# Kernel optimization log

Measured on AMD Instinct MI355X. Metric: run time of the kernel, lower is better.

## Reference

```python
import jax, jax.numpy as jnp
import numpy as np

B, N_SRC, N_NGH, D, H = 256, 32, 2048, 128, 2
DK = D // H  # 64
FEAT = 128
NEG_INF = -1e10
LN_EPS = 1e-5


def setup_inputs() -> dict:
    key = jax.random.key(0)
    ks = jax.random.split(key, 16)
    inp = {
        "src": jax.random.normal(ks[0], (B, N_SRC, D), jnp.float32),
        "ngh_feat": jax.random.normal(ks[1], (B * N_NGH, D), jnp.float32),
        "hidden": jnp.zeros((B * N_NGH, D), jnp.float32),
        "mask": jax.random.bernoulli(ks[2], 0.5, (B, N_NGH)),
        # GRUCell params (torch layout: [3H, in], gate order r,z,n)
        "gru_w_ih": jax.random.normal(ks[3], (3 * D, D), jnp.float32) * 0.05,
        "gru_w_hh": jax.random.normal(ks[4], (3 * D, D), jnp.float32) * 0.05,
        "gru_b_ih": jnp.zeros((3 * D,), jnp.float32),
        "gru_b_hh": jnp.zeros((3 * D,), jnp.float32),
        # multi-head attention projections (no bias in source)
        "w_qs": jax.random.normal(ks[5], (H * DK, D), jnp.float32) * np.sqrt(2.0 / (D + DK)).astype(np.float32),
        "w_ks": jax.random.normal(ks[6], (H * DK, D), jnp.float32) * np.sqrt(2.0 / (D + DK)).astype(np.float32),
        "w_vs": jax.random.normal(ks[7], (H * DK, D), jnp.float32) * np.sqrt(2.0 / (D + DK)).astype(np.float32),
        "fc_w": jax.random.normal(ks[8], (D, H * DK), jnp.float32) * 0.05,
        "fc_b": jnp.zeros((D,), jnp.float32),
        "ln_g": jnp.ones((D,), jnp.float32),
        "ln_b": jnp.zeros((D,), jnp.float32),
        # MergeLayer(model_dim, model_dim, feat_dim, feat_dim)
        "m_fc1_w": jax.random.normal(ks[9], (FEAT, 2 * D), jnp.float32) * 0.05,
        "m_fc1_b": jnp.zeros((FEAT,), jnp.float32),
        "m_fc2_w": jax.random.normal(ks[10], (FEAT, FEAT), jnp.float32) * 0.05,
        "m_fc2_b": jnp.zeros((FEAT,), jnp.float32),
    }
    return inp


def gru_cell(x, h, w_ih, w_hh, b_ih, b_hh):
    gi = x @ w_ih.T + b_ih
    gh = h @ w_hh.T + b_hh
    ir, iz, in_ = jnp.split(gi, 3, axis=-1)
    hr, hz, hn = jnp.split(gh, 3, axis=-1)
    r = jax.nn.sigmoid(ir + hr)
    z = jax.nn.sigmoid(iz + hz)
    n = jnp.tanh(in_ + r * hn)
    return (1.0 - z) * n + z * h


def reference(src, ngh_feat, hidden, mask,
              gru_w_ih, gru_w_hh, gru_b_ih, gru_b_hh,
              w_qs, w_ks, w_vs, fc_w, fc_b, ln_g, ln_b,
              m_fc1_w, m_fc1_b, m_fc2_w, m_fc2_b):
    b, n_src, d = src.shape
    n_ngh = mask.shape[1]
    nn = n_ngh // n_src  # neighbors per source
    temperature = jnp.sqrt(jnp.float32(DK))

    # GRU walk encoding of neighbor features -> seq [B, N_ngh, D]
    seq = gru_cell(ngh_feat, hidden, gru_w_ih, gru_w_hh, gru_b_ih, gru_b_hh)
    seq = seq.reshape(b, n_ngh, d)

    # grouped multi-head attention (q per source, k/v over its nn neighbors)
    q = (src @ w_qs.T).reshape(b, n_src, H, DK)            # bshd
    k = (seq @ w_ks.T).reshape(b, n_src, nn, H, DK)        # bsnhd
    v = (seq @ w_vs.T).reshape(b, n_src, nn, H, DK)
    scores = jnp.einsum('bshd,bsnhd->bshn', q, k) / temperature
    m = mask.reshape(b, n_src, 1, nn)                      # broadcast over heads
    scores = jnp.where(m, NEG_INF, scores)
    attn = jax.nn.softmax(scores, axis=-1)                 # dropout is eval no-op
    out = jnp.einsum('bshn,bsnhd->bshd', attn, v).reshape(b, n_src, H * DK)
    out = out @ fc_w.T + fc_b

    # residual + layernorm
    x = out + src
    mu = jnp.mean(x, axis=-1, keepdims=True)
    var = jnp.var(x, axis=-1, keepdims=True)
    x = (x - mu) * jax.lax.rsqrt(var + LN_EPS) * ln_g + ln_b

    # MergeLayer: cat + MLP
    cat = jnp.concatenate([x, src], axis=-1)
    h1 = jax.nn.relu(cat @ m_fc1_w.T + m_fc1_b)
    z = h1 @ m_fc2_w.T + m_fc2_b                            # [B, N_src, feat_dim]
    return z
```

## Files before the change

kernel.cpp:

```cpp
#include <hip/hip_runtime.h>

typedef float  f32x4  __attribute__((ext_vector_type(4)));
typedef short  bf16x8 __attribute__((ext_vector_type(8)));
typedef unsigned short u16x4 __attribute__((ext_vector_type(4)));

typedef const __attribute__((address_space(1))) unsigned int* gas_u32;
typedef __attribute__((address_space(3))) unsigned int* las_u32;

#define MFMA16(a,b,c) __builtin_amdgcn_mfma_f32_16x16x32_bf16((a),(b),(c),0,0,0)

__device__ __forceinline__ unsigned short f2bf(float f){
  unsigned u = __float_as_uint(f);
  u += 0x7fffu + ((u>>16)&1u);
  return (unsigned short)(u>>16);
}
__device__ __forceinline__ float bf2f(unsigned short u){
  return __uint_as_float(((unsigned)u)<<16);
}
__device__ __forceinline__ float sigm(float x){
  return __fdividef(1.f, 1.f + __expf(-x));
}
__device__ __forceinline__ float tanhfast(float x){
  return 1.f - __fdividef(2.f, __expf(2.f*x) + 1.f);
}
__device__ __forceinline__ float dot128(const float* __restrict__ w, const float* s){
  float a0=0.f,a1=0.f,a2=0.f,a3=0.f;
  #pragma unroll
  for (int e=0;e<32;++e){
    f32x4 w4 = *(const f32x4*)(w + (e<<2));
    f32x4 x4 = *(const f32x4*)(s + (e<<2));
    a0 = fmaf(w4[0],x4[0],a0); a1 = fmaf(w4[1],x4[1],a1);
    a2 = fmaf(w4[2],x4[2],a2); a3 = fmaf(w4[3],x4[3],a3);
  }
  return (a0+a1)+(a2+a3);
}
__device__ __forceinline__ bf16x8 cvt8(const f32x4 a, const f32x4 b){
  union { int i[4]; bf16x8 v; } u;
  asm("v_cvt_pk_bf16_f32 %0, %1, %2" : "=v"(u.i[0]) : "v"(a[0]), "v"(a[1]));
  asm("v_cvt_pk_bf16_f32 %0, %1, %2" : "=v"(u.i[1]) : "v"(a[2]), "v"(a[3]));
  asm("v_cvt_pk_bf16_f32 %0, %1, %2" : "=v"(u.i[2]) : "v"(b[0]), "v"(b[1]));
  asm("v_cvt_pk_bf16_f32 %0, %1, %2" : "=v"(u.i[3]) : "v"(b[2]), "v"(b[3]));
  return u.v;
}
__device__ __forceinline__ int swx(int m){ return (((m&7)<<1) | ((m>>3)&1)) << 2; }
__device__ __forceinline__ int sws(int m){ return ((m&7)<<3) | (((m>>3)&1)<<6); }

#define XB_OFF   0
#define SEQ_OFF  32768
#define QK_OFF   49152
#define SC_OFF   53248
#define SH_OFF   53760
#define BIAS_OFF 57856
#define SMEM_SZ  59904

__global__ void prep_all(const float* __restrict__ wih, const float* __restrict__ whh,
                         const float* __restrict__ wqs, const float* __restrict__ wks,
                         const float* __restrict__ wvs, const float* __restrict__ fcw,
                         const float* __restrict__ src, const int* __restrict__ mask_i,
                         const float* __restrict__ hid,
                         unsigned short* __restrict__ wbf, float* __restrict__ M_ws,
                         unsigned short* __restrict__ qk_ws,
                         unsigned long long* __restrict__ mask_bits,
                         int* __restrict__ flags){
  __shared__ __align__(16) float sl_src[32*128];
  __shared__ __align__(16) float sl_q[32*128];
  const int b = blockIdx.x, t = threadIdx.x;
  if (b < 384){
    const int tid = b*256 + t;
    if (tid < 49152) wbf[tid] = f2bf(wih[tid]);
    else             wbf[tid] = f2bf(whh[tid-49152]);
  } else if (b < 512){
    const int tid = (b-384)*256 + t;
    const int h = tid>>14, d = (tid>>7)&127, e = tid&127;
    float a = 0.f;
    for (int j=0;j<64;++j)
      a = fmaf(fcw[d*128 + (h<<6) + j], wvs[((h<<6)+j)*128 + e], a);
    M_ws[tid] = a;
  } else if (b < 768){
    const int blk = b - 512;
    const size_t s0 = (size_t)blk * 32;
    for (int i=0;i<16;++i) sl_src[t + i*256] = src[s0*128 + t + i*256];
    __syncthreads();
    for (int k=0;k<16;++k){
      const int job = t + k*256, s = job>>7, c = job&127;
      sl_q[job] = dot128(wqs + c*128, sl_src + s*128);
    }
    __syncthreads();
    const int d = t&127, h = (t>>7)&1;
    float acc[32];
    #pragma unroll
    for (int s=0;s<32;++s) acc[s]=0.f;
    for (int j=0;j<64;++j){
      const float wk = wks[((h<<6)+j)*128 + d];
      #pragma unroll
      for (int s=0;s<32;++s) acc[s] = fmaf(wk, sl_q[s*128 + (h<<6) + j], acc[s]);
    }
    for (int s=0;s<32;++s) qk_ws[(s0+s)*256 + (h<<7) + d] = f2bf(acc[s]);
  } else if (b < 2816){
    const int blk = b - 768;
    const int wv = t>>6, lane = t&63;
    const int gsrc = blk*4 + wv;
    const unsigned v = (unsigned)mask_i[(size_t)gsrc*64 + lane];
    const int bytemode = __any((int)(v > 1u));
    bool bit;
    if (bytemode) bit = (((const unsigned char*)mask_i)[(size_t)gsrc*64 + lane] != 0);
    else          bit = (v != 0u);
    const unsigned long long bits = __ballot((int)bit);
    if (lane == 0) mask_bits[gsrc] = bits;
  } else {
    const size_t blk = b - 2816;
    bool nz = false;
    #pragma unroll 4
    for (int it=0; it<32; ++it){
      const size_t idx = blk*8192 + (size_t)it*256 + t;
      const f32x4 v = *(const f32x4*)(hid + idx*4);
      nz = nz || (v[0]!=0.f)||(v[1]!=0.f)||(v[2]!=0.f)||(v[3]!=0.f);
    }
    if (__ballot((int)nz)){ if ((t&63)==0) atomicOr(flags+1, 1); }
  }
}

__device__ __forceinline__ void scores_pv(char* smem, int srcI, unsigned long long mb,
                                          int wv, int lane){
  const unsigned short* seq = (const unsigned short*)(smem + SEQ_OFF);
  const float* qk_lds = (const float*)(smem + QK_OFF);
  float* sc = (float*)(smem + SC_OFF);
  float* sH = (float*)(smem + SH_OFF);
  {
    const int hh = wv & 1;
    const float* qrow = qk_lds + (srcI<<8) + (hh<<7);
    float a = 0.f;
    #pragma unroll
    for (int c8=0; c8<16; ++c8){
      const int cb = c8<<3;
      bf16x8 kc = *(const bf16x8*)&seq[(lane<<7) + (cb ^ sws(lane))];
      #pragma unroll
      for (int u=0;u<8;++u) a = fmaf(bf2f((unsigned short)kc[u]), qrow[cb+u], a);
    }
    float s = ((mb>>lane)&1ull) ? -1e10f : a*0.125f;
    float mx = s;
    #pragma unroll
    for (int o=32;o>=1;o>>=1) mx = fmaxf(mx, __shfl_xor(mx,o));
    const float e = __expf(s - mx);
    float sum = e;
    #pragma unroll
    for (int o=32;o>=1;o>>=1) sum += __shfl_xor(sum,o);
    if (wv < 2) sc[(hh<<6)+lane] = __fdividef(e, sum);
  }
  asm volatile("s_waitcnt lgkmcnt(0)" ::: "memory");
  __builtin_amdgcn_sched_barrier(0);
  __builtin_amdgcn_s_barrier();
  {
    const int tt = (wv<<6)+lane;
    const int jidx = tt>>2, sub = tt&3;
    const int hh2 = jidx>>5, quad = jidx&31;
    f32x4 a = {0.f,0.f,0.f,0.f};
    #pragma unroll
    for (int i=0;i<16;++i){
      const int rr = (sub<<4)+i;
      const u16x4 sv = *(const u16x4*)&seq[(rr<<7) + ((quad<<2) ^ sws(rr))];
      const float w = sc[(hh2<<6)+rr];
      #pragma unroll
      for (int k=0;k<4;++k) a[k] = fmaf(w, bf2f(sv[k]), a[k]);
    }
    #pragma unroll
    for (int k=0;k<4;++k) a[k] += __shfl_xor(a[k],1);
    #pragma unroll
    for (int k=0;k<4;++k) a[k] += __shfl_xor(a[k],2);
    if (sub == 0)
      *(f32x4*)&sH[(((srcI<<1)+hh2)<<7) + (quad<<2)] = a;
  }
}

__global__ __attribute__((amdgpu_flat_work_group_size(256,256)))
           __attribute__((amdgpu_waves_per_eu(2)))
void cawn_main(
    const float* __restrict__ src, const float* __restrict__ ngh,
    const float* __restrict__ hid,
    const float* __restrict__ bih, const float* __restrict__ bhh,
    const float* __restrict__ fcb, const float* __restrict__ lng,
    const float* __restrict__ lnb, const float* __restrict__ m1w,
    const float* __restrict__ m1b, const float* __restrict__ m2w,
    const float* __restrict__ m2b,
    const unsigned short* __restrict__ wihb, const unsigned short* __restrict__ whhb,
    const float* __restrict__ M_ws, const unsigned short* __restrict__ qk_ws,
    const unsigned long long* __restrict__ mask_bits,
    const int* __restrict__ flags, float* __restrict__ out)
{
  __shared__ __align__(16) char smem[SMEM_SZ];
  float* qk_lds = (float*)(smem + QK_OFF);
  float* brz0   = (float*)(smem + BIAS_OFF);
  float* brz1   = (float*)(smem + BIAS_OFF + 512);
  float* bin_l  = (float*)(smem + BIAS_OFF + 1024);
  float* bhn_l  = (float*)(smem + BIAS_OFF + 1536);
  unsigned short* seq = (unsigned short*)(smem + SEQ_OFF);

  const int t    = threadIdx.x;
  const int wv   = t >> 6;
  const int lane = t & 63;
  const int l15  = lane & 15;
  const int lgrp = lane >> 4;
  const int gsrc0 = blockIdx.x * 4;
  const f32x4 z4 = {0.f,0.f,0.f,0.f};
  const int hz = flags[1];

  if (t < 128){
    brz0[t]  = bih[t]     + bhh[t];
    brz1[t]  = bih[128+t] + bhh[128+t];
    bin_l[t] = bih[256+t];
    bhn_l[t] = bhh[256+t];
  }
  #pragma unroll
  for (int s=0;s<4;++s)
    qk_lds[(s<<8)+t] = bf2f(qk_ws[(size_t)(gsrc0+s)*256 + t]);
  const unsigned long long mb0 = mask_bits[gsrc0];
  const unsigned long long mb1 = mask_bits[gsrc0+1];
  const unsigned long long mb2 = mask_bits[gsrc0+2];
  const unsigned long long mb3 = mask_bits[gsrc0+3];

  if (!hz){
    bf16x8 Wf[3][2][4];
    #pragma unroll
    for (int g=0; g<3; ++g)
      #pragma unroll
      for (int j=0; j<2; ++j){
        const int nc = (wv<<5) + (j<<4) + l15;
        #pragma unroll
        for (int kb=0; kb<4; ++kb)
          Wf[g][j][kb] = *(const bf16x8*)(wihb + (((g<<7) + nc)<<7) + (kb<<5) + (lgrp<<3));
      }

    auto issue = [&](int kk){
      const int srcI = kk>>2, stg = kk&3;
      const size_t base = (size_t)(gsrc0+srcI)*8192 + (size_t)stg*2048;
      #pragma unroll
      for (int r=0;r<2;++r){
        const int rl = (wv<<2) + (r<<1) + (lane>>5);
        const int s16 = (lane&31) ^ (((rl&7)<<1) | ((rl>>3)&1));
        const float* g = ngh + base + (rl<<7) + (s16<<2);
        char* l = smem + XB_OFF + (kk&3)*8192 + (((wv<<2)+(r<<1))<<9);
        __builtin_amdgcn_global_load_lds((gas_u32)g, (las_u32)l, 16, 0, 0);
      }
    };
    issue(0); issue(1);

    for (int k=0;k<16;++k){
      if (k < 14) issue(k+2);
      if (k < 14)      asm volatile("s_waitcnt vmcnt(4) lgkmcnt(0)" ::: "memory");
      else if (k==14)  asm volatile("s_waitcnt vmcnt(2) lgkmcnt(0)" ::: "memory");
      else             asm volatile("s_waitcnt vmcnt(0) lgkmcnt(0)" ::: "memory");
      __builtin_amdgcn_sched_barrier(0);
      __builtin_amdgcn_s_barrier();

      const int srcI = k>>2, stg = k&3;
      const float* xrow = (const float*)(smem + XB_OFF + (k&3)*8192) + (l15<<7);
      const int sw = swx(l15);
      bf16x8 bx[4];
      #pragma unroll
      for (int kb=0;kb<4;++kb){
        const int c0 = (kb<<5) + (lgrp<<3);
        const f32x4 u0 = *(const f32x4*)&xrow[c0 ^ sw];
        const f32x4 u1 = *(const f32x4*)&xrow[(c0+4) ^ sw];
        bx[kb] = cvt8(u0,u1);
      }
      f32x4 ar[2]={z4,z4}, az[2]={z4,z4}, an[2]={z4,z4};
      #pragma unroll
      for (int j=0;j<2;++j)
        #pragma unroll
        for (int kb=0;kb<4;++kb){
          ar[j] = MFMA16(Wf[0][j][kb], bx[kb], ar[j]);
          az[j] = MFMA16(Wf[1][j][kb], bx[kb], az[j]);
          an[j] = MFMA16(Wf[2][j][kb], bx[kb], an[j]);
        }
      const int mrow = (stg<<4) + l15;
      #pragma unroll
      for (int j=0;j<2;++j){
        const int colb = (wv<<5) + (j<<4) + (lgrp<<2);
        const f32x4 b0 = *(const f32x4*)&brz0[colb];
        const f32x4 b1 = *(const f32x4*)&brz1[colb];
        const f32x4 b2 = *(const f32x4*)&bin_l[colb];
        const f32x4 b3 = *(const f32x4*)&bhn_l[colb];
        u16x4 sq;
        #pragma unroll
        for (int i=0;i<4;++i){
          const float rv = sigm(ar[j][i] + b0[i]);
          const float zv = sigm(az[j][i] + b1[i]);
          const float nv = tanhfast(an[j][i] + b2[i] + rv*b3[i]);
          sq[i] = f2bf((1.f - zv)*nv);
        }
        *(u16x4*)&seq[(mrow<<7) + (colb ^ sws(mrow))] = sq;
      }

      if (stg == 3){
        asm volatile("s_waitcnt lgkmcnt(0)" ::: "memory");
        __builtin_amdgcn_sched_barrier(0);
        __builtin_amdgcn_s_barrier();
        const unsigned long long mb = (srcI==0)?mb0:(srcI==1)?mb1:(srcI==2)?mb2:mb3;
        scores_pv(smem, srcI, mb, wv, lane);
      }
    }
  } else {
    float* xb0 = (float*)(smem + XB_OFF);
    float* xb1 = (float*)(smem + XB_OFF + 8192);
    for (int srcI=0;srcI<4;++srcI){
      const int gsrc = gsrc0+srcI;
      for (int stg=0;stg<4;++stg){
        #pragma unroll
        for (int it=0; it<2; ++it){
          const int f = t + (it<<8);
          const int m = f>>5, c0 = (f&31)<<2;
          const int sw = swx(m);
          const size_t gb = (size_t)gsrc*8192 + stg*2048 + (m<<7) + c0;
          *(f32x4*)&xb0[(m<<7)+(c0^sw)] = *(const f32x4*)(ngh+gb);
          *(f32x4*)&xb1[(m<<7)+(c0^sw)] = *(const f32x4*)(hid+gb);
        }
        __syncthreads();
        const float* xrow = xb0 + (l15<<7);
        const float* hrow = xb1 + (l15<<7);
        const int sw = swx(l15);
        bf16x8 bx[4], bh[4];
        #pragma unroll
        for (int kb=0;kb<4;++kb){
          const int c0 = (kb<<5) + (lgrp<<3);
          bx[kb] = cvt8(*(const f32x4*)&xrow[c0 ^ sw], *(const f32x4*)&xrow[(c0+4) ^ sw]);
          bh[kb] = cvt8(*(const f32x4*)&hrow[c0 ^ sw], *(const f32x4*)&hrow[(c0+4) ^ sw]);
        }
        f32x4 ar[2]={z4,z4}, az[2]={z4,z4}, an[2]={z4,z4}, anh[2]={z4,z4};
        #pragma unroll
        for (int j=0;j<2;++j){
          const int nc = (wv<<5)+(j<<4)+l15;
          #pragma unroll
          for (int kb=0;kb<4;++kb){
            const int ko=(kb<<5)+(lgrp<<3);
            bf16x8 w0 = *(const bf16x8*)(wihb + ((      nc)<<7) + ko);
            bf16x8 w1 = *(const bf16x8*)(wihb + (((128)+nc)<<7) + ko);
            bf16x8 w2 = *(const bf16x8*)(wihb + (((256)+nc)<<7) + ko);
            ar[j] = MFMA16(w0, bx[kb], ar[j]);
            az[j] = MFMA16(w1, bx[kb], az[j]);
            an[j] = MFMA16(w2, bx[kb], an[j]);
            bf16x8 u0 = *(const bf16x8*)(whhb + ((      nc)<<7) + ko);
            bf16x8 u1 = *(const bf16x8*)(whhb + (((128)+nc)<<7) + ko);
            bf16x8 u2 = *(const bf16x8*)(whhb + (((256)+nc)<<7) + ko);
            ar[j]  = MFMA16(u0, bh[kb], ar[j]);
            az[j]  = MFMA16(u1, bh[kb], az[j]);
            anh[j] = MFMA16(u2, bh[kb], anh[j]);
          }
        }
        const int mrow = (stg<<4) + l15;
        #pragma unroll
        for (int j=0;j<2;++j){
          const int colb = (wv<<5) + (j<<4) + (lgrp<<2);
          const f32x4 b0 = *(const f32x4*)&brz0[colb];
          const f32x4 b1 = *(const f32x4*)&brz1[colb];
          const f32x4 b2 = *(const f32x4*)&bin_l[colb];
          const f32x4 b3 = *(const f32x4*)&bhn_l[colb];
          const f32x4 hv = *(const f32x4*)&hrow[colb ^ sw];
          u16x4 sq;
          #pragma unroll
          for (int i=0;i<4;++i){
            const float rv = sigm(ar[j][i] + b0[i]);
            const float zv = sigm(az[j][i] + b1[i]);
            const float nv = tanhfast(an[j][i] + b2[i] + rv*(anh[j][i] + b3[i]));
            sq[i] = f2bf((1.f - zv)*nv + zv*hv[i]);
          }
          *(u16x4*)&seq[(mrow<<7) + (colb ^ sws(mrow))] = sq;
        }
        __syncthreads();
      }
      const unsigned long long mb = (srcI==0)?mb0:(srcI==1)?mb1:(srcI==2)?mb2:mb3;
      scores_pv(smem, srcI, mb, wv, lane);
      __syncthreads();
    }
  }

  __syncthreads();
  float* ep1  = (float*)smem;
  float* ep2  = (float*)(smem + 2048);
  float* srce = (float*)(smem + 4096);
  float* sH   = (float*)(smem + SH_OFF);
  srce[t]     = src[(size_t)gsrc0*128 + t];
  srce[t+256] = src[(size_t)gsrc0*128 + t + 256];
  __syncthreads();

  const int d  = t & 127;
  const int sh = (t >> 7) << 1;
  #pragma unroll
  for (int si=0; si<2; ++si){
    const int s = sh + si;
    float a = fcb[d];
    a += dot128(M_ws +         d*128, &sH[((s<<1)  )<<7]);
    a += dot128(M_ws + 16384 + d*128, &sH[((s<<1)+1)<<7]);
    ep1[s*128+d] = a + srce[s*128+d];
  }
  __syncthreads();
  {
    const int s = wv;
    const float v0 = ep1[s*128+lane], v1 = ep1[s*128+64+lane];
    float sum = v0+v1, sq_ = v0*v0 + v1*v1;
    #pragma unroll
    for (int o=32;o>=1;o>>=1){ sum += __shfl_xor(sum,o); sq_ += __shfl_xor(sq_,o); }
    const float mu  = sum * 0.0078125f;
    const float var = sq_ * 0.0078125f - mu*mu;
    const float rs  = rsqrtf(var + 1e-5f);
    ep1[s*128+lane]    = (v0-mu)*rs*lng[lane]    + lnb[lane];
    ep1[s*128+64+lane] = (v1-mu)*rs*lng[64+lane] + lnb[64+lane];
  }
  __syncthreads();
  #pragma unroll
  for (int si=0; si<2; ++si){
    const int s = sh + si;
    float a = m1b[d];
    a += dot128(m1w + d*256,       ep1  + s*128);
    a += dot128(m1w + d*256 + 128, srce + s*128);
    ep2[s*128+d] = fmaxf(a, 0.f);
  }
  __syncthreads();
  #pragma unroll
  for (int si=0; si<2; ++si){
    const int s = sh + si;
    out[(size_t)(gsrc0+s)*128 + d] = m2b[d] + dot128(m2w + d*128, ep2 + s*128);
  }
}

extern "C" void kernel_launch(void* const* d_in, const int* in_sizes, int n_in,
                              void* d_out, int out_size, void* d_ws, size_t ws_size,
                              hipStream_t stream){
  const float* src = (const float*)d_in[0];
  const float* ngh = (const float*)d_in[1];
  const float* hid = (const float*)d_in[2];
  const int*   msk = (const int*)  d_in[3];
  const float* wih = (const float*)d_in[4];
  const float* whh = (const float*)d_in[5];
  const float* bih = (const float*)d_in[6];
  const float* bhh = (const float*)d_in[7];
  const float* wqs = (const float*)d_in[8];
  const float* wks = (const float*)d_in[9];
  const float* wvs = (const float*)d_in[10];
  const float* fcw = (const float*)d_in[11];
  const float* fcb = (const float*)d_in[12];
  const float* lng = (const float*)d_in[13];
  const float* lnb = (const float*)d_in[14];
  const float* m1w = (const float*)d_in[15];
  const float* m1b = (const float*)d_in[16];
  const float* m2w = (const float*)d_in[17];
  const float* m2b = (const float*)d_in[18];
  float* out = (float*)d_out;

  unsigned short* wbf   = (unsigned short*)d_ws;
  int*            flags = (int*)((char*)d_ws + 196608);
  float*          M_ws  = (float*)((char*)d_ws + 196672);
  unsigned short* qk_ws = (unsigned short*)((char*)d_ws + 327744);
  unsigned long long* mask_bits = (unsigned long long*)((char*)d_ws + 4522048);

  hipMemsetAsync((char*)d_ws + 196608, 0, 64, stream);
  prep_all <<<4864, 256, 0, stream>>>(wih, whh, wqs, wks, wvs, fcw, src, msk, hid,
                                      wbf, M_ws, qk_ws, mask_bits, flags);
  cawn_main<<<2048, 256, 0, stream>>>(src, ngh, hid, bih, bhh,
                                      fcb, lng, lnb, m1w, m1b, m2w, m2b,
                                      wbf, wbf + 49152, M_ws, qk_ws,
                                      mask_bits, flags, out);
}
```

Baseline: 456.3 us.

## Shrink LDS to triple-buffered prefetch, MFMA scores, bf16 qk for higher occupancy

Changes the neighbor-feature prefetch ring from four 8KB slots to three, issuing the next load after the barrier. It keeps qk in LDS as bf16 with the 1/8 temperature folded into prep, and computes attention scores with MFMA instead of scalar dot products. It also packs GRU outputs with hardware bf16 conversion and raises waves_per_eu to 3. The aim is to cut LDS footprint and register pressure so more workgroups fit per CU, at the cost of a shallower prefetch ring and bf16 rounding of q·Wk.

Measured after the change: 526.8 us. 1.15x slower.

```diff
diff --git a/kernel.cpp b/kernel.cpp
--- a/kernel.cpp
+++ b/kernel.cpp
@@ -42,16 +42,22 @@
   asm("v_cvt_pk_bf16_f32 %0, %1, %2" : "=v"(u.i[3]) : "v"(b[2]), "v"(b[3]));
   return u.v;
 }
+__device__ __forceinline__ u16x4 pack4(float a, float b, float c, float d){
+  union { int i[2]; u16x4 v; } u;
+  asm("v_cvt_pk_bf16_f32 %0, %1, %2" : "=v"(u.i[0]) : "v"(a), "v"(b));
+  asm("v_cvt_pk_bf16_f32 %0, %1, %2" : "=v"(u.i[1]) : "v"(c), "v"(d));
+  return u.v;
+}
 __device__ __forceinline__ int swx(int m){ return (((m&7)<<1) | ((m>>3)&1)) << 2; }
 __device__ __forceinline__ int sws(int m){ return ((m&7)<<3) | (((m>>3)&1)<<6); }
 
 #define XB_OFF   0
-#define SEQ_OFF  32768
-#define QK_OFF   49152
-#define SC_OFF   53248
-#define SH_OFF   53760
-#define BIAS_OFF 57856
-#define SMEM_SZ  59904
+#define SEQ_OFF  24576
+#define QKB_OFF  40960
+#define SC_OFF   43008
+#define SH_OFF   43520
+#define BIAS_OFF 47616
+#define SMEM_SZ  49664
 
 __global__ void prep_all(const float* __restrict__ wih, const float* __restrict__ whh,
                          const float* __restrict__ wqs, const float* __restrict__ wks,
@@ -95,7 +101,7 @@
       #pragma unroll
       for (int s=0;s<32;++s) acc[s] = fmaf(wk, sl_q[s*128 + (h<<6) + j], acc[s]);
     }
-    for (int s=0;s<32;++s) qk_ws[(s0+s)*256 + (h<<7) + d] = f2bf(acc[s]);
+    for (int s=0;s<32;++s) qk_ws[(s0+s)*256 + (h<<7) + d] = f2bf(acc[s]*0.125f);
   } else if (b < 2816){
     const int blk = b - 768;
     const int wv = t>>6, lane = t&63;
@@ -121,23 +127,32 @@
 }
 
 __device__ __forceinline__ void scores_pv(char* smem, int srcI, unsigned long long mb,
-                                          int wv, int lane){
-  const unsigned short* seq = (const unsigned short*)(smem + SEQ_OFF);
-  const float* qk_lds = (const float*)(smem + QK_OFF);
+                                          int wv, int lane, int l15, int lgrp){
+  unsigned short* seq = (unsigned short*)(smem + SEQ_OFF);
+  const unsigned short* qkb = (const unsigned short*)(smem + QKB_OFF);
   float* sc = (float*)(smem + SC_OFF);
   float* sH = (float*)(smem + SH_OFF);
+  const f32x4 z4 = {0.f,0.f,0.f,0.f};
   {
-    const int hh = wv & 1;
-    const float* qrow = qk_lds + (srcI<<8) + (hh<<7);
-    float a = 0.f;
-    #pragma unroll
-    for (int c8=0; c8<16; ++c8){
-      const int cb = c8<<3;
-      bf16x8 kc = *(const bf16x8*)&seq[(lane<<7) + (cb ^ sws(lane))];
-      #pragma unroll
-      for (int u=0;u<8;++u) a = fmaf(bf2f((unsigned short)kc[u]), qrow[cb+u], a);
-    }
-    float s = ((mb>>lane)&1ull) ? -1e10f : a*0.125f;
+    const int srow = (wv<<4) + l15;
+    f32x4 s4 = z4;
+    #pragma unroll
+    for (int kb=0;kb<4;++kb){
+      const int ko = (kb<<5) + (lgrp<<3);
+      bf16x8 qa = *(const bf16x8*)&qkb[(srcI<<8) + ((l15&1)<<7) + ko];
+      bf16x8 sb = *(const bf16x8*)&seq[(srow<<7) + (ko ^ sws(srow))];
+      s4 = MFMA16(qa, sb, s4);
+    }
+    if (lgrp == 0){
+      sc[      (wv<<4) + l15] = s4[0];
+      sc[64 +  (wv<<4) + l15] = s4[1];
+    }
+  }
+  asm volatile("s_waitcnt lgkmcnt(0)" ::: "memory");
+  __builtin_amdgcn_sched_barrier(0);
+  __builtin_amdgcn_s_barrier();
+  if (wv < 2){
+    float s = ((mb>>lane)&1ull) ? -1e10f : sc[(wv<<6)+lane];
     float mx = s;
     #pragma unroll
     for (int o=32;o>=1;o>>=1) mx = fmaxf(mx, __shfl_xor(mx,o));
@@ -145,16 +160,16 @@
     float sum = e;
     #pragma unroll
     for (int o=32;o>=1;o>>=1) sum += __shfl_xor(sum,o);
-    if (wv < 2) sc[(hh<<6)+lane] = __fdividef(e, sum);
+    sc[(wv<<6)+lane] = __fdividef(e, sum);
   }
   asm volatile("s_waitcnt lgkmcnt(0)" ::: "memory");
   __builtin_amdgcn_sched_barrier(0);
   __builtin_amdgcn_s_barrier();
   {
-    const int tt = (wv<<6)+lane;
+    const int tt = (wv<<6) + lane;
     const int jidx = tt>>2, sub = tt&3;
     const int hh2 = jidx>>5, quad = jidx&31;
-    f32x4 a = {0.f,0.f,0.f,0.f};
+    f32x4 a = z4;
     #pragma unroll
     for (int i=0;i<16;++i){
       const int rr = (sub<<4)+i;
@@ -173,7 +188,7 @@
 }
 
 __global__ __attribute__((amdgpu_flat_work_group_size(256,256)))
-           __attribute__((amdgpu_waves_per_eu(2)))
+           __attribute__((amdgpu_waves_per_eu(3)))
 void cawn_main(
     const float* __restrict__ src, const float* __restrict__ ngh,
     const float* __restrict__ hid,
@@ -188,12 +203,12 @@
     const int* __restrict__ flags, float* __restrict__ out)
 {
   __shared__ __align__(16) char smem[SMEM_SZ];
-  float* qk_lds = (float*)(smem + QK_OFF);
   float* brz0   = (float*)(smem + BIAS_OFF);
   float* brz1   = (float*)(smem + BIAS_OFF + 512);
   float* bin_l  = (float*)(smem + BIAS_OFF + 1024);
   float* bhn_l  = (float*)(smem + BIAS_OFF + 1536);
   unsigned short* seq = (unsigned short*)(smem + SEQ_OFF);
+  unsigned short* qkb = (unsigned short*)(smem + QKB_OFF);
 
   const int t    = threadIdx.x;
   const int wv   = t >> 6;
@@ -212,7 +227,7 @@
   }
   #pragma unroll
   for (int s=0;s<4;++s)
-    qk_lds[(s<<8)+t] = bf2f(qk_ws[(size_t)(gsrc0+s)*256 + t]);
+    qkb[(s<<8)+t] = qk_ws[(size_t)(gsrc0+s)*256 + t];
   const unsigned long long mb0 = mask_bits[gsrc0];
   const unsigned long long mb1 = mask_bits[gsrc0+1];
   const unsigned long long mb2 = mask_bits[gsrc0+2];
@@ -230,7 +245,7 @@
           Wf[g][j][kb] = *(const bf16x8*)(wihb + (((g<<7) + nc)<<7) + (kb<<5) + (lgrp<<3));
       }
 
-    auto issue = [&](int kk){
+    auto issue = [&](int kk, int rbuf){
       const int srcI = kk>>2, stg = kk&3;
       const size_t base = (size_t)(gsrc0+srcI)*8192 + (size_t)stg*2048;
       #pragma unroll
@@ -238,22 +253,25 @@
         const int rl = (wv<<2) + (r<<1) + (lane>>5);
         const int s16 = (lane&31) ^ (((rl&7)<<1) | ((rl>>3)&1));
         const float* g = ngh + base + (rl<<7) + (s16<<2);
-        char* l = smem + XB_OFF + (kk&3)*8192 + (((wv<<2)+(r<<1))<<9);
+        char* l = smem + XB_OFF + rbuf*8192 + (((wv<<2)+(r<<1))<<9);
         __builtin_amdgcn_global_load_lds((gas_u32)g, (las_u32)l, 16, 0, 0);
       }
     };
-    issue(0); issue(1);
-
+    issue(0,0); issue(1,1);
+
+    int rb = 0;
     for (int k=0;k<16;++k){
-      if (k < 14) issue(k+2);
-      if (k < 14)      asm volatile("s_waitcnt vmcnt(4) lgkmcnt(0)" ::: "memory");
-      else if (k==14)  asm volatile("s_waitcnt vmcnt(2) lgkmcnt(0)" ::: "memory");
-      else             asm volatile("s_waitcnt vmcnt(0) lgkmcnt(0)" ::: "memory");
+      if (k < 15) asm volatile("s_waitcnt vmcnt(2) lgkmcnt(0)" ::: "memory");
+      else        asm volatile("s_waitcnt vmcnt(0) lgkmcnt(0)" ::: "memory");
       __builtin_amdgcn_sched_barrier(0);
       __builtin_amdgcn_s_barrier();
+      if (k+2 < 16){
+        int ri = rb+2; if (ri>=3) ri-=3;
+        issue(k+2, ri);
+      }
 
       const int srcI = k>>2, stg = k&3;
-      const float* xrow = (const float*)(smem + XB_OFF + (k&3)*8192) + (l15<<7);
+      const float* xrow = (const float*)(smem + XB_OFF + rb*8192) + (l15<<7);
       const int sw = swx(l15);
       bf16x8 bx[4];
       #pragma unroll
@@ -280,15 +298,15 @@
         const f32x4 b1 = *(const f32x4*)&brz1[colb];
         const f32x4 b2 = *(const f32x4*)&bin_l[colb];
         const f32x4 b3 = *(const f32x4*)&bhn_l[colb];
-        u16x4 sq;
+        float o[4];
         #pragma unroll
         for (int i=0;i<4;++i){
           const float rv = sigm(ar[j][i] + b0[i]);
           const float zv = sigm(az[j][i] + b1[i]);
           const float nv = tanhfast(an[j][i] + b2[i] + rv*b3[i]);
-          sq[i] = f2bf((1.f - zv)*nv);
-        }
-        *(u16x4*)&seq[(mrow<<7) + (colb ^ sws(mrow))] = sq;
+          o[i] = (1.f - zv)*nv;
+        }
+        *(u16x4*)&seq[(mrow<<7) + (colb ^ sws(mrow))] = pack4(o[0],o[1],o[2],o[3]);
       }
 
       if (stg == 3){
@@ -296,8 +314,9 @@
         __builtin_amdgcn_sched_barrier(0);
         __builtin_amdgcn_s_barrier();
         const unsigned long long mb = (srcI==0)?mb0:(srcI==1)?mb1:(srcI==2)?mb2:mb3;
-        scores_pv(smem, srcI, mb, wv, lane);
-      }
+        scores_pv(smem, srcI, mb, wv, lane, l15, lgrp);
+      }
+      rb = (rb+1 == 3) ? 0 : rb+1;
     }
   } else {
     float* xb0 = (float*)(smem + XB_OFF);
@@ -355,20 +374,20 @@
           const f32x4 b2 = *(const f32x4*)&bin_l[colb];
           const f32x4 b3 = *(const f32x4*)&bhn_l[colb];
           const f32x4 hv = *(const f32x4*)&hrow[colb ^ sw];
-          u16x4 sq;
+          float o[4];
           #pragma unroll
           for (int i=0;i<4;++i){
             const float rv = sigm(ar[j][i] + b0[i]);
             const float zv = sigm(az[j][i] + b1[i]);
             const float nv = tanhfast(an[j][i] + b2[i] + rv*(anh[j][i] + b3[i]));
-            sq[i] = f2bf((1.f - zv)*nv + zv*hv[i]);
+            o[i] = (1.f - zv)*nv + zv*hv[i];
           }
-          *(u16x4*)&seq[(mrow<<7) + (colb ^ sws(mrow))] = sq;
+          *(u16x4*)&seq[(mrow<<7) + (colb ^ sws(mrow))] = pack4(o[0],o[1],o[2],o[3]);
         }
         __syncthreads();
       }
       const unsigned long long mb = (srcI==0)?mb0:(srcI==1)?mb1:(srcI==2)?mb2:mb3;
-      scores_pv(smem, srcI, mb, wv, lane);
+      scores_pv(smem, srcI, mb, wv, lane, l15, lgrp);
       __syncthreads();
     }
   }
```
